# Kernel optimization log

Hardware: AMD Instinct MI355X
Metric: run time of the kernel (lower is better)

## Reference

```python
import math
import jax, jax.numpy as jnp
import numpy as np

S, D, E = 8192, 2048, 64            # tokens, model_dim, num_experts
CAPACITY_FACTOR = 1.0
CAP = int(CAPACITY_FACTOR * math.ceil(S / E))  # 128, static (training-mode 'drop' gate)


def setup_inputs() -> dict:
    key = jax.random.key(0)
    kx, kw = jax.random.split(key)
    x = jax.random.normal(kx, (S, D), dtype=jnp.float32)
    wg = jax.random.normal(kw, (E, D), dtype=jnp.float32) * 0.02  # Linear(D, E, bias=False) weight
    return {"x": x, "wg": wg}


def reference(x, wg):
    # logits = self.wg(input)
    logits = jnp.einsum('sd,ed->se', x, wg)                 # [S, E]
    gates = jax.nn.softmax(logits, axis=1)                  # [S, E]
    indices1_s = jnp.argmax(gates, axis=1)                  # [S]
    mask1 = jax.nn.one_hot(indices1_s, E, dtype=gates.dtype)  # [S, E]

    # load-balancing aux loss
    me = jnp.mean(gates, axis=0)
    ce = jnp.mean(mask1, axis=0)
    l_aux = jnp.mean(me * ce) * (E * E)

    # gates1_s computed BEFORE capacity drop (as in source)
    gates1_s = jnp.sum(gates * mask1, axis=1)               # [S]

    # fused_cumsum_sub_one: position of each token within its expert's queue
    locations1 = jnp.cumsum(mask1, axis=0) - 1.0            # [S, E]
    # capacity drop ('drop' gate type)
    mask1 = mask1 * (locations1 < CAP).astype(mask1.dtype)
    locations1_s = jnp.sum(locations1 * mask1, axis=1).astype(jnp.int32)  # [S]

    gates1 = gates1_s[:, None] * mask1                      # [S, E]
    locations1_sc = jax.nn.one_hot(locations1_s, CAP, dtype=gates1.dtype)  # [S, CAP]
    # bmm(gates1[:,:,None], loc_sc[:,None,:]) == outer product per token
    combine1_sec = jnp.einsum('se,sc->sec', gates1, locations1_sc)  # [S, E, CAP]
    dispatch_mask = combine1_sec.astype(bool)
    return l_aux, combine1_sec, dispatch_mask
```

## Files before the change

kernel.cpp:

```cpp
#include <hip/hip_runtime.h>
#include <cstddef>
#include <cstdint>

#define S_TOK 8192
#define DDIM  2048
#define NEXP  64
#define CAPTY 128
#define KC    64
#define TPB   64
#define NBLK  (S_TOK / TPB)
#define SPLITK 8
#define KPER  (DDIM / SPLITK)
#define SEC   (S_TOK * NEXP * CAPTY)

__global__ __launch_bounds__(256)
void fill_zero_kernel(float* __restrict__ out)
{
    const size_t n4 = (size_t)SEC / 2;
    float4* out4 = (float4*)out;
    size_t i = (size_t)blockIdx.x * 256 + threadIdx.x;
    const size_t stride = (size_t)gridDim.x * 256;
    float4 z = make_float4(0.f, 0.f, 0.f, 0.f);
    for (size_t idx = i; idx < n4; idx += stride)
        out4[idx] = z;
    if (i == 0) out[(size_t)2 * SEC] = 0.0f;
}

__global__ __launch_bounds__(256)
void gate_gemm_kernel(const float* __restrict__ x, const float* __restrict__ wg,
                      float* __restrict__ part)
{
    __shared__ float xs[KC][TPB + 2];
    __shared__ float ws[KC][NEXP];

    const int tid = threadIdx.x;
    const int e4  = tid & 15;
    const int tg  = tid >> 4;
    const int kp  = blockIdx.x & (SPLITK - 1);
    const int tc  = blockIdx.x >> 3;
    const int t_base = tc * TPB;
    const int k_base = kp * KPER;

    float acc[4][4];
#pragma unroll
    for (int i = 0; i < 4; ++i)
#pragma unroll
        for (int j = 0; j < 4; ++j) acc[i][j] = 0.0f;

    for (int kc0 = 0; kc0 < KPER; kc0 += KC) {
        const int kc = k_base + kc0;
        __syncthreads();
#pragma unroll
        for (int m = 0; m < 4; ++m) {
            int idx = tid + 256 * m;
            int t = idx & 63;
            int c = idx >> 6;
            float4 v = *(const float4*)(x + (size_t)(t_base + t) * DDIM + kc + c * 4);
            xs[c * 4 + 0][t] = v.x;
            xs[c * 4 + 1][t] = v.y;
            xs[c * 4 + 2][t] = v.z;
            xs[c * 4 + 3][t] = v.w;
            float4 w = *(const float4*)(wg + (size_t)t * DDIM + kc + c * 4);
            ws[c * 4 + 0][t] = w.x;
            ws[c * 4 + 1][t] = w.y;
            ws[c * 4 + 2][t] = w.z;
            ws[c * 4 + 3][t] = w.w;
        }
        __syncthreads();
#pragma unroll 8
        for (int k = 0; k < KC; ++k) {
            float4 wv = *(const float4*)&ws[k][e4 * 4];
            float2 xa = *(const float2*)&xs[k][tg * 4];
            float2 xb = *(const float2*)&xs[k][tg * 4 + 2];
            float xv0 = xa.x, xv1 = xa.y, xv2 = xb.x, xv3 = xb.y;
            acc[0][0] += xv0 * wv.x; acc[0][1] += xv0 * wv.y;
            acc[0][2] += xv0 * wv.z; acc[0][3] += xv0 * wv.w;
            acc[1][0] += xv1 * wv.x; acc[1][1] += xv1 * wv.y;
            acc[1][2] += xv1 * wv.z; acc[1][3] += xv1 * wv.w;
            acc[2][0] += xv2 * wv.x; acc[2][1] += xv2 * wv.y;
            acc[2][2] += xv2 * wv.z; acc[2][3] += xv2 * wv.w;
            acc[3][0] += xv3 * wv.x; acc[3][1] += xv3 * wv.y;
            acc[3][2] += xv3 * wv.z; acc[3][3] += xv3 * wv.w;
        }
    }

#pragma unroll
    for (int i = 0; i < 4; ++i) {
        float4 v = make_float4(acc[i][0], acc[i][1], acc[i][2], acc[i][3]);
        *(float4*)(part + ((size_t)kp * S_TOK + t_base + tg * 4 + i) * NEXP + e4 * 4) = v;
    }
}

__global__ __launch_bounds__(64)
void softmax_kernel(const float* __restrict__ part,
                    float* __restrict__ gate_s, int* __restrict__ expert,
                    int* __restrict__ rank, int* __restrict__ hist,
                    float* __restrict__ partial_g)
{
    __shared__ float probs[TPB][NEXP + 1];
    __shared__ int   sexp[TPB];

    const int t   = threadIdx.x;
    const int tok = blockIdx.x * TPB + t;

    float lg[NEXP];
#pragma unroll
    for (int e = 0; e < NEXP; e += 4) {
        float4 v = *(const float4*)(part + (size_t)tok * NEXP + e);
        lg[e] = v.x; lg[e + 1] = v.y; lg[e + 2] = v.z; lg[e + 3] = v.w;
    }
#pragma unroll
    for (int kp = 1; kp < SPLITK; ++kp) {
#pragma unroll
        for (int e = 0; e < NEXP; e += 4) {
            float4 v = *(const float4*)(part + ((size_t)kp * S_TOK + tok) * NEXP + e);
            lg[e] += v.x; lg[e + 1] += v.y; lg[e + 2] += v.z; lg[e + 3] += v.w;
        }
    }

    float m = -1e30f; int am = 0;
#pragma unroll
    for (int e = 0; e < NEXP; ++e)
        if (lg[e] > m) { m = lg[e]; am = e; }
    float s = 0.0f;
#pragma unroll
    for (int e = 0; e < NEXP; ++e) { float p = __expf(lg[e] - m); lg[e] = p; s += p; }
    float rcp = 1.0f / s;
#pragma unroll
    for (int e = 0; e < NEXP; ++e) probs[t][e] = lg[e] * rcp;

    sexp[t] = am;
    gate_s[tok] = rcp;
    expert[tok] = am;
    __syncthreads();

    int r = 0;
    for (int u = 0; u < t; ++u) r += (sexp[u] == am) ? 1 : 0;
    rank[tok] = r;

    {
        int e = t;
        float pg = 0.0f; int cnt = 0;
        for (int u = 0; u < TPB; ++u) {
            pg  += probs[u][e];
            cnt += (sexp[u] == e) ? 1 : 0;
        }
        partial_g[blockIdx.x * NEXP + e] = pg;
        hist[blockIdx.x * NEXP + e]      = cnt;
    }
}

__global__ __launch_bounds__(64)
void scan_kernel(const int* __restrict__ hist, const float* __restrict__ partial_g,
                 int* __restrict__ chunk_base, float* __restrict__ out)
{
    int e = threadIdx.x;
    int base = 0;
    float sg = 0.0f;
    for (int c = 0; c < NBLK; ++c) {
        chunk_base[c * NEXP + e] = base;
        base += hist[c * NEXP + e];
        sg   += partial_g[c * NEXP + e];
    }
    float v = sg * (float)base;
#pragma unroll
    for (int off = 32; off > 0; off >>= 1) v += __shfl_down(v, off);
    if (e == 0)
        out[0] = v * (64.0f / (8192.0f * 8192.0f));
}

__global__ __launch_bounds__(256)
void scatter_kernel(const float* __restrict__ gate_s, const int* __restrict__ expert,
                    const int* __restrict__ rank, const int* __restrict__ chunk_base,
                    float* __restrict__ out)
{
    int s = blockIdx.x * 256 + threadIdx.x;
    if (s >= S_TOK) return;
    int e   = expert[s];
    int loc = chunk_base[(s >> 6) * NEXP + e] + rank[s];
    if (loc < CAPTY) {
        size_t idx = 1 + (size_t)s * (NEXP * CAPTY) + (size_t)e * CAPTY + loc;
        out[idx]       = gate_s[s];
        out[idx + SEC] = 1.0f;
    }
}

extern "C" void kernel_launch(void* const* d_in, const int* in_sizes, int n_in,
                              void* d_out, int out_size, void* d_ws, size_t ws_size,
                              hipStream_t stream)
{
    const float* x  = (const float*)d_in[0];
    const float* wg = (const float*)d_in[1];
    float* out = (float*)d_out;
    char* ws = (char*)d_ws;

    float* part      = (float*)(ws + 0);
    size_t off = (size_t)SPLITK * S_TOK * NEXP * sizeof(float);
    float* gate_s    = (float*)(ws + off);          off += 32768;
    int*   expert    = (int*)  (ws + off);          off += 32768;
    int*   rank      = (int*)  (ws + off);          off += 32768;
    int*   hist      = (int*)  (ws + off);          off += 32768;
    int*   chunk_b   = (int*)  (ws + off);          off += 32768;
    float* partial_g = (float*)(ws + off);

    fill_zero_kernel<<<4096, 256, 0, stream>>>(out);
    gate_gemm_kernel<<<NBLK * SPLITK, 256, 0, stream>>>(x, wg, part);
    softmax_kernel<<<NBLK, 64, 0, stream>>>(part, gate_s, expert, rank, hist, partial_g);
    scan_kernel<<<1, 64, 0, stream>>>(hist, partial_g, chunk_b, out);
    scatter_kernel<<<(S_TOK + 255) / 256, 256, 0, stream>>>(gate_s, expert, rank, chunk_b, out);
}
```

Measured before the change: 630.8 us.

## Fuse zero-fill, gate GEMM and softmax into one interleaved kernel

Merges the output zero-fill, split-K gate GEMM and softmax into a single launch where every fifth block does GEMM work and the rest zero the output. The last split-K block per token chunk, detected via an atomic counter, reduces partials and runs softmax, argmax, rank and histogram. Scan and scatter are merged into one single-block kernel. The aim is to overlap the compute with the bandwidth-bound fill and cut launch overhead, at the cost of an extra memset, atomics, and GEMM reads contending with fill writes.

```diff
diff --git a/kernel.cpp b/kernel.cpp
--- a/kernel.cpp
+++ b/kernel.cpp
@@ -11,35 +11,46 @@
 #define NBLK  (S_TOK / TPB)
 #define SPLITK 8
 #define KPER  (DDIM / SPLITK)
-#define SEC   (S_TOK * NEXP * CAPTY)
+#define SEC   ((size_t)S_TOK * NEXP * CAPTY)
+#define NGEMM (NBLK * SPLITK)
+#define NFILL 4096
+#define NTOT  (NGEMM + NFILL)
+
+struct GemmSm { float xs[KC][TPB + 2]; float ws2[KC][NEXP]; };
+struct SoftSm { float probs[TPB][NEXP + 1]; int sexp[TPB]; };
+union SMemU { GemmSm g; SoftSm s; };
 
 __global__ __launch_bounds__(256)
-void fill_zero_kernel(float* __restrict__ out)
+void fused_kernel(const float* __restrict__ x, const float* __restrict__ wg,
+                  float* __restrict__ part, float* __restrict__ gate_s,
+                  int* __restrict__ expert, int* __restrict__ rank,
+                  int* __restrict__ hist, float* __restrict__ partial_g,
+                  int* __restrict__ done, float* __restrict__ out)
 {
-    const size_t n4 = (size_t)SEC / 2;
-    float4* out4 = (float4*)out;
-    size_t i = (size_t)blockIdx.x * 256 + threadIdx.x;
-    const size_t stride = (size_t)gridDim.x * 256;
-    float4 z = make_float4(0.f, 0.f, 0.f, 0.f);
-    for (size_t idx = i; idx < n4; idx += stride)
-        out4[idx] = z;
-    if (i == 0) out[(size_t)2 * SEC] = 0.0f;
-}
-
-__global__ __launch_bounds__(256)
-void gate_gemm_kernel(const float* __restrict__ x, const float* __restrict__ wg,
-                      float* __restrict__ part)
-{
-    __shared__ float xs[KC][TPB + 2];
-    __shared__ float ws[KC][NEXP];
-
+    __shared__ SMemU sm;
+    __shared__ int s_old;
     const int tid = threadIdx.x;
-    const int e4  = tid & 15;
-    const int tg  = tid >> 4;
-    const int kp  = blockIdx.x & (SPLITK - 1);
-    const int tc  = blockIdx.x >> 3;
+    const int bid = blockIdx.x;
+
+    if (bid % 5 != 0) {
+        const size_t fidx = (size_t)(bid - bid / 5 - 1);
+        const size_t n4 = (size_t)2 * SEC / 4;
+        float4* out4 = (float4*)out;
+        size_t i = fidx * 256 + tid;
+        const size_t stride = (size_t)NFILL * 256;
+        float4 z = make_float4(0.f, 0.f, 0.f, 0.f);
+        for (size_t idx = i; idx < n4; idx += stride) out4[idx] = z;
+        if (i == 0) out[2 * SEC] = 0.0f;
+        return;
+    }
+
+    const int g  = bid / 5;
+    const int kp = g & (SPLITK - 1);
+    const int tc = g >> 3;
     const int t_base = tc * TPB;
     const int k_base = kp * KPER;
+    const int e4 = tid & 15;
+    const int tg = tid >> 4;
 
     float acc[4][4];
 #pragma unroll
@@ -56,22 +67,22 @@
             int t = idx & 63;
             int c = idx >> 6;
             float4 v = *(const float4*)(x + (size_t)(t_base + t) * DDIM + kc + c * 4);
-            xs[c * 4 + 0][t] = v.x;
-            xs[c * 4 + 1][t] = v.y;
-            xs[c * 4 + 2][t] = v.z;
-            xs[c * 4 + 3][t] = v.w;
+            sm.g.xs[c * 4 + 0][t] = v.x;
+            sm.g.xs[c * 4 + 1][t] = v.y;
+            sm.g.xs[c * 4 + 2][t] = v.z;
+            sm.g.xs[c * 4 + 3][t] = v.w;
             float4 w = *(const float4*)(wg + (size_t)t * DDIM + kc + c * 4);
-            ws[c * 4 + 0][t] = w.x;
-            ws[c * 4 + 1][t] = w.y;
-            ws[c * 4 + 2][t] = w.z;
-            ws[c * 4 + 3][t] = w.w;
+            sm.g.ws2[c * 4 + 0][t] = w.x;
+            sm.g.ws2[c * 4 + 1][t] = w.y;
+            sm.g.ws2[c * 4 + 2][t] = w.z;
+            sm.g.ws2[c * 4 + 3][t] = w.w;
         }
         __syncthreads();
 #pragma unroll 8
         for (int k = 0; k < KC; ++k) {
-            float4 wv = *(const float4*)&ws[k][e4 * 4];
-            float2 xa = *(const float2*)&xs[k][tg * 4];
-            float2 xb = *(const float2*)&xs[k][tg * 4 + 2];
+            float4 wv = *(const float4*)&sm.g.ws2[k][e4 * 4];
+            float2 xa = *(const float2*)&sm.g.xs[k][tg * 4];
+            float2 xb = *(const float2*)&sm.g.xs[k][tg * 4 + 2];
             float xv0 = xa.x, xv1 = xa.y, xv2 = xb.x, xv3 = xb.y;
             acc[0][0] += xv0 * wv.x; acc[0][1] += xv0 * wv.y;
             acc[0][2] += xv0 * wv.z; acc[0][3] += xv0 * wv.w;
@@ -89,99 +100,100 @@
         float4 v = make_float4(acc[i][0], acc[i][1], acc[i][2], acc[i][3]);
         *(float4*)(part + ((size_t)kp * S_TOK + t_base + tg * 4 + i) * NEXP + e4 * 4) = v;
     }
+
+    __threadfence();
+    __syncthreads();
+    if (tid == 0) s_old = atomicAdd(&done[tc], 1);
+    __syncthreads();
+    if (s_old != SPLITK - 1) return;
+    __threadfence();
+
+    {
+        const int t = tid >> 2, q = tid & 3;
+        const int tok = t_base + t;
+#pragma unroll
+        for (int jj = 0; jj < 4; ++jj) {
+            float4 a = make_float4(0.f, 0.f, 0.f, 0.f);
+#pragma unroll
+            for (int kpp = 0; kpp < SPLITK; ++kpp) {
+                float4 v = *(const float4*)(part + ((size_t)kpp * S_TOK + tok) * NEXP + q * 16 + jj * 4);
+                a.x += v.x; a.y += v.y; a.z += v.z; a.w += v.w;
+            }
+            sm.s.probs[t][q * 16 + jj * 4 + 0] = a.x;
+            sm.s.probs[t][q * 16 + jj * 4 + 1] = a.y;
+            sm.s.probs[t][q * 16 + jj * 4 + 2] = a.z;
+            sm.s.probs[t][q * 16 + jj * 4 + 3] = a.w;
+        }
+        __syncthreads();
+
+        if (tid < TPB) {
+            const int t2 = tid, tok2 = t_base + t2;
+            float m = -1e30f; int am = 0;
+            for (int e = 0; e < NEXP; ++e) {
+                float v = sm.s.probs[t2][e];
+                if (v > m) { m = v; am = e; }
+            }
+            float s = 0.0f;
+            for (int e = 0; e < NEXP; ++e) s += __expf(sm.s.probs[t2][e] - m);
+            float rcp = 1.0f / s;
+            for (int e = 0; e < NEXP; ++e)
+                sm.s.probs[t2][e] = __expf(sm.s.probs[t2][e] - m) * rcp;
+            sm.s.sexp[t2] = am;
+            gate_s[tok2] = rcp;
+            expert[tok2] = am;
+        }
+        __syncthreads();
+
+        if (tid < TPB) {
+            const int t2 = tid;
+            const int am = sm.s.sexp[t2];
+            int r = 0;
+            for (int u = 0; u < t2; ++u) r += (sm.s.sexp[u] == am) ? 1 : 0;
+            rank[t_base + t2] = r;
+        } else if (tid < 2 * TPB) {
+            const int e = tid - TPB;
+            float pg = 0.0f; int cnt = 0;
+            for (int u = 0; u < TPB; ++u) {
+                pg  += sm.s.probs[u][e];
+                cnt += (sm.s.sexp[u] == e) ? 1 : 0;
+            }
+            partial_g[tc * NEXP + e] = pg;
+            hist[tc * NEXP + e]      = cnt;
+        }
+    }
 }
 
-__global__ __launch_bounds__(64)
-void softmax_kernel(const float* __restrict__ part,
-                    float* __restrict__ gate_s, int* __restrict__ expert,
-                    int* __restrict__ rank, int* __restrict__ hist,
-                    float* __restrict__ partial_g)
+__global__ __launch_bounds__(256)
+void scan_scatter_kernel(const int* __restrict__ hist, const float* __restrict__ partial_g,
+                         const float* __restrict__ gate_s, const int* __restrict__ expert,
+                         const int* __restrict__ rank, float* __restrict__ out)
 {
-    __shared__ float probs[TPB][NEXP + 1];
-    __shared__ int   sexp[TPB];
-
-    const int t   = threadIdx.x;
-    const int tok = blockIdx.x * TPB + t;
-
-    float lg[NEXP];
-#pragma unroll
-    for (int e = 0; e < NEXP; e += 4) {
-        float4 v = *(const float4*)(part + (size_t)tok * NEXP + e);
-        lg[e] = v.x; lg[e + 1] = v.y; lg[e + 2] = v.z; lg[e + 3] = v.w;
-    }
-#pragma unroll
-    for (int kp = 1; kp < SPLITK; ++kp) {
-#pragma unroll
-        for (int e = 0; e < NEXP; e += 4) {
-            float4 v = *(const float4*)(part + ((size_t)kp * S_TOK + tok) * NEXP + e);
-            lg[e] += v.x; lg[e + 1] += v.y; lg[e + 2] += v.z; lg[e + 3] += v.w;
-        }
-    }
-
-    float m = -1e30f; int am = 0;
-#pragma unroll
-    for (int e = 0; e < NEXP; ++e)
-        if (lg[e] > m) { m = lg[e]; am = e; }
-    float s = 0.0f;
-#pragma unroll
-    for (int e = 0; e < NEXP; ++e) { float p = __expf(lg[e] - m); lg[e] = p; s += p; }
-    float rcp = 1.0f / s;
-#pragma unroll
-    for (int e = 0; e < NEXP; ++e) probs[t][e] = lg[e] * rcp;
-
-    sexp[t] = am;
-    gate_s[tok] = rcp;
-    expert[tok] = am;
+    __shared__ int base_s[NBLK][NEXP];
+    const int tid = threadIdx.x;
+
+    if (tid < NEXP) {
+        const int e = tid;
+        int base = 0; float sg = 0.0f;
+        for (int c = 0; c < NBLK; ++c) {
+            base_s[c][e] = base;
+            base += hist[c * NEXP + e];
+            sg  += partial_g[c * NEXP + e];
+        }
+        float v = sg * (float)base;
+#pragma unroll
+        for (int off = 32; off > 0; off >>= 1) v += __shfl_down(v, off);
+        if (e == 0) out[0] = v * (64.0f / (8192.0f * 8192.0f));
+    }
     __syncthreads();
 
-    int r = 0;
-    for (int u = 0; u < t; ++u) r += (sexp[u] == am) ? 1 : 0;
-    rank[tok] = r;
-
-    {
-        int e = t;
-        float pg = 0.0f; int cnt = 0;
-        for (int u = 0; u < TPB; ++u) {
-            pg  += probs[u][e];
-            cnt += (sexp[u] == e) ? 1 : 0;
-        }
-        partial_g[blockIdx.x * NEXP + e] = pg;
-        hist[blockIdx.x * NEXP + e]      = cnt;
-    }
-}
-
-__global__ __launch_bounds__(64)
-void scan_kernel(const int* __restrict__ hist, const float* __restrict__ partial_g,
-                 int* __restrict__ chunk_base, float* __restrict__ out)
-{
-    int e = threadIdx.x;
-    int base = 0;
-    float sg = 0.0f;
-    for (int c = 0; c < NBLK; ++c) {
-        chunk_base[c * NEXP + e] = base;
-        base += hist[c * NEXP + e];
-        sg   += partial_g[c * NEXP + e];
-    }
-    float v = sg * (float)base;
-#pragma unroll
-    for (int off = 32; off > 0; off >>= 1) v += __shfl_down(v, off);
-    if (e == 0)
-        out[0] = v * (64.0f / (8192.0f * 8192.0f));
-}
-
-__global__ __launch_bounds__(256)
-void scatter_kernel(const float* __restrict__ gate_s, const int* __restrict__ expert,
-                    const int* __restrict__ rank, const int* __restrict__ chunk_base,
-                    float* __restrict__ out)
-{
-    int s = blockIdx.x * 256 + threadIdx.x;
-    if (s >= S_TOK) return;
-    int e   = expert[s];
-    int loc = chunk_base[(s >> 6) * NEXP + e] + rank[s];
-    if (loc < CAPTY) {
-        size_t idx = 1 + (size_t)s * (NEXP * CAPTY) + (size_t)e * CAPTY + loc;
-        out[idx]       = gate_s[s];
-        out[idx + SEC] = 1.0f;
+    for (int s = tid; s < S_TOK; s += 256) {
+        const int e = expert[s];
+        const int loc = base_s[s >> 6][e] + rank[s];
+        if (loc < CAPTY) {
+            size_t idx = 1 + (size_t)s * (NEXP * CAPTY) + (size_t)e * CAPTY + loc;
+            out[idx]       = gate_s[s];
+            out[idx + SEC] = 1.0f;
+        }
     }
 }
 
@@ -200,12 +212,12 @@
     int*   expert    = (int*)  (ws + off);          off += 32768;
     int*   rank      = (int*)  (ws + off);          off += 32768;
     int*   hist      = (int*)  (ws + off);          off += 32768;
-    int*   chunk_b   = (int*)  (ws + off);          off += 32768;
-    float* partial_g = (float*)(ws + off);
-
-    fill_zero_kernel<<<4096, 256, 0, stream>>>(out);
-    gate_gemm_kernel<<<NBLK * SPLITK, 256, 0, stream>>>(x, wg, part);
-    softmax_kernel<<<NBLK, 64, 0, stream>>>(part, gate_s, expert, rank, hist, partial_g);
-    scan_kernel<<<1, 64, 0, stream>>>(hist, partial_g, chunk_b, out);
-    scatter_kernel<<<(S_TOK + 255) / 256, 256, 0, stream>>>(gate_s, expert, rank, chunk_b, out);
+    float* partial_g = (float*)(ws + off);          off += 32768;
+    int*   done      = (int*)  (ws + off);
+
+    hipMemsetAsync(done, 0, NBLK * sizeof(int), stream);
+
+    fused_kernel<<<NTOT, 256, 0, stream>>>(x, wg, part, gate_s, expert, rank,
+                                           hist, partial_g, done, out);
+    scan_scatter_kernel<<<1, 256, 0, stream>>>(hist, partial_g, gate_s, expert, rank, out);
 }
```

Result: slower. 907.5 us (+43.9%).
